# Kernel tuning notes

Measured on AMD Instinct MI355X. Metric: run time of the kernel, lower is better.

The kernel has to match this reference:

```python
import jax, jax.numpy as jnp
import numpy as np

B, HI, WI, CV, CT, T = 8, 64, 64, 512, 512, 77
HH, DH = 8, 64
TOP_M, TOPP, CLAMP_LOGIT, TAU, ALPHA0 = 5, 0.9, 2.0, 0.5, 0.1


def setup_inputs() -> dict:
    key = jax.random.key(0)
    ks = jax.random.split(key, 12)
    s = 0.02
    w = lambda k, shp: jax.random.normal(k, shp, jnp.float32) * s
    return {
        "visual": jax.random.normal(ks[0], (B, HI, WI, CV), jnp.float32),
        "text": jax.random.normal(ks[1], (B, T, CT), jnp.float32),
        "ln1_g": jnp.ones((CV,), jnp.float32), "ln1_b": jnp.zeros((CV,), jnp.float32),
        "ln2_g": jnp.ones((CV,), jnp.float32), "ln2_b": jnp.zeros((CV,), jnp.float32),
        "Wq": w(ks[2], (CV, CV)), "bq": jnp.zeros((CV,), jnp.float32),
        "Wk": w(ks[3], (CT, CV)), "bk": jnp.zeros((CV,), jnp.float32),
        "Wv": w(ks[4], (CT, CV)), "bv": jnp.zeros((CV,), jnp.float32),
        "Wo": w(ks[5], (CV, CV)), "bo": jnp.zeros((CV,), jnp.float32),
        "Wg": w(ks[6], (CV, 1)), "bg": jnp.zeros((1,), jnp.float32),
        "W1": w(ks[7], (CV, 4 * CV)), "b1": jnp.zeros((4 * CV,), jnp.float32),
        "W2": w(ks[8], (4 * CV, CV)), "b2": jnp.zeros((CV,), jnp.float32),
        "logit_scale": jnp.asarray(np.log(1.0 / 0.07), jnp.float32),
        "alpha": jnp.asarray(ALPHA0, jnp.float32),
    }


def _ln(x, g, b, eps=1e-5):
    m = x.mean(-1, keepdims=True)
    v = ((x - m) ** 2).mean(-1, keepdims=True)
    return (x - m) * jax.lax.rsqrt(v + eps) * g + b


def _l2norm(t, eps=1e-6):  # F.normalize: x / max(||x||, eps)
    return t / jnp.maximum(jnp.linalg.norm(t, axis=-1, keepdims=True), eps)


def _sam_forward(visual, text, ln1_g, ln1_b, ln2_g, ln2_b, Wq, bq, Wk, bk, Wv, bv,
                 Wo, bo, Wg, bg, W1, b1, W2, b2, logit_scale, alpha):
    Bx, Hi, Wi, C = visual.shape
    N = Hi * Wi
    x = _ln(visual, ln1_g, ln1_b).reshape(Bx, N, C)          # pre-LN, [B,N,Cv]
    q_full = x @ Wq + bq
    k_full = text @ Wk + bk
    v_full = text @ Wv + bv
    pad = jnp.abs(text).sum(-1) <= 1e-6                      # [B,T] all-zero tokens
    q = _l2norm(q_full).reshape(Bx, N, HH, DH)               # normalize over full Cv, then split heads
    k = _l2norm(k_full).reshape(Bx, -1, HH, DH)
    v = v_full.reshape(Bx, -1, HH, DH)
    scale = jnp.exp(jnp.clip(logit_scale, -CLAMP_LOGIT, CLAMP_LOGIT)) / jnp.sqrt(jnp.float32(DH))
    sim = jnp.einsum("bnhd,bthd->bnht", q, k) * scale        # [B,N,H,T]
    sim = jnp.where(pad[:, None, None, :], -jnp.inf, sim)
    # top-m sparsify (keep entries >= kth largest)
    if TOP_M < sim.shape[-1]:
        kth = jax.lax.top_k(sim, TOP_M)[0][..., -1:]
        sim = jnp.where(sim >= kth, sim, -jnp.inf)
    attn = jax.nn.softmax(sim, axis=-1)
    # top-p nucleus: sort desc, keep cum<=p (always keep top-1), scatter back, renorm
    idx = jnp.argsort(-attn, axis=-1)
    prob = jnp.take_along_axis(attn, idx, axis=-1)
    keep = (jnp.cumsum(prob, axis=-1) <= TOPP).astype(attn.dtype)
    keep = keep.at[..., 0].set(1.0)
    inv = jnp.argsort(idx, axis=-1)
    sparse = jnp.take_along_axis(keep * prob, inv, axis=-1)
    attn = sparse / jnp.maximum(sparse.sum(-1, keepdims=True), 1e-6)
    # entropy-based confidence, [B,N,1]
    ah = attn.transpose(0, 2, 1, 3)                          # [B,H,N,T]
    maxp = ah.max(-1, keepdims=True)
    t_eff = jnp.maximum((ah > 0).astype(attn.dtype).sum(-1, keepdims=True), 1.0)
    denom = jnp.log(jnp.maximum(t_eff, 2.0))
    pc = jnp.maximum(ah, 1e-8)
    entropy = -(pc * jnp.log(pc)).sum(-1, keepdims=True) / denom
    conf = jnp.clip(maxp * (1.0 - entropy), 0.0, 1.0).mean(axis=1)
    aligned = jnp.einsum("bnht,bthd->bnhd", attn, v).reshape(Bx, N, C)
    aligned = aligned @ Wo + bo
    # trust region: cap ||aligned|| at tau * rms(x)
    x_rms = jnp.sqrt((x ** 2).mean(-1, keepdims=True)) + 1e-6
    a_norm = jnp.sqrt((aligned ** 2).sum(-1, keepdims=True))
    aligned = aligned * jnp.minimum(TAU * x_rms / jnp.maximum(a_norm, 1e-6), 1.0)
    gate = jax.nn.sigmoid(x @ Wg + bg) * conf
    y = x + alpha * gate * aligned
    h = jax.nn.gelu(_ln(y, ln2_g, ln2_b) @ W1 + b1, approximate=False)
    y = y + (h @ W2 + b2)
    return y.reshape(Bx, Hi, Wi, C)


def reference(visual, text, ln1_g, ln1_b, ln2_g, ln2_b, Wq, bq, Wk, bk, Wv, bv,
              Wo, bo, Wg, bg, W1, b1, W2, b2, logit_scale, alpha):
    return _sam_forward(visual, text, ln1_g, ln1_b, ln2_g, ln2_b, Wq, bq, Wk, bk,
                        Wv, bv, Wo, bo, Wg, bg, W1, b1, W2, b2, logit_scale, alpha)
```

## Files before the change

### kernel.cpp

```cpp
#include <hip/hip_runtime.h>
#include <hip/hip_bf16.h>
#include <math.h>

#define NROW 32768
#define CVC  512
#define T77  77
#define BT   616
#define HHC  8
#define DHC  64

typedef __attribute__((ext_vector_type(8))) short bf16x8;
typedef __attribute__((ext_vector_type(4))) float f32x4;

__device__ __forceinline__ void gload_lds16(const void* g, void* l) {
  __builtin_amdgcn_global_load_lds(
      (__attribute__((address_space(1))) void*)g,
      (__attribute__((address_space(3))) void*)l, 16, 0, 0);
}

__device__ __forceinline__ float wave_reduce_sum(float v) {
  #pragma unroll
  for (int s = 32; s > 0; s >>= 1) v += __shfl_xor(v, s, 64);
  return v;
}

__global__ __launch_bounds__(256)
void stats1_kernel(const float* __restrict__ visual, const float* __restrict__ g,
                   const float* __restrict__ b, const float* __restrict__ Wg,
                   const float* __restrict__ bg,
                   float* __restrict__ mean1, float* __restrict__ rstd1,
                   float* __restrict__ xrms, float* __restrict__ gpre,
                   __hip_bfloat16* __restrict__ xbf) {
  const int lane = threadIdx.x & 63;
  const int row  = blockIdx.x * 4 + (threadIdx.x >> 6);
  const float* vr = visual + (size_t)row * CVC + lane * 8;
  float4 va = *(const float4*)vr;
  float4 vb = *(const float4*)(vr + 4);
  float v[8] = {va.x, va.y, va.z, va.w, vb.x, vb.y, vb.z, vb.w};
  float s = 0.f;
  #pragma unroll
  for (int i = 0; i < 8; i++) s += v[i];
  float m = wave_reduce_sum(s) * (1.0f / CVC);
  float s2 = 0.f;
  #pragma unroll
  for (int i = 0; i < 8; i++) { float d = v[i] - m; s2 += d * d; }
  float rs = rsqrtf(wave_reduce_sum(s2) * (1.0f / CVC) + 1e-5f);
  const float4 g0 = *(const float4*)(g + lane * 8), g1v = *(const float4*)(g + lane * 8 + 4);
  const float4 b0 = *(const float4*)(b + lane * 8), b1v = *(const float4*)(b + lane * 8 + 4);
  const float4 w0 = *(const float4*)(Wg + lane * 8), w1 = *(const float4*)(Wg + lane * 8 + 4);
  float gg[8] = {g0.x, g0.y, g0.z, g0.w, g1v.x, g1v.y, g1v.z, g1v.w};
  float bb[8] = {b0.x, b0.y, b0.z, b0.w, b1v.x, b1v.y, b1v.z, b1v.w};
  float ww[8] = {w0.x, w0.y, w0.z, w0.w, w1.x, w1.y, w1.z, w1.w};
  float x[8], sx2 = 0.f, sg = 0.f;
  union { bf16x8 v8; __hip_bfloat16 h[8]; } u;
  #pragma unroll
  for (int i = 0; i < 8; i++) {
    x[i] = (v[i] - m) * rs * gg[i] + bb[i];
    sx2 += x[i] * x[i];
    sg  += x[i] * ww[i];
    u.h[i] = __float2bfloat16(x[i]);
  }
  *(bf16x8*)(xbf + (size_t)row * CVC + lane * 8) = u.v8;
  sx2 = wave_reduce_sum(sx2);
  sg  = wave_reduce_sum(sg);
  if (lane == 0) {
    mean1[row] = m; rstd1[row] = rs;
    xrms[row] = sqrtf(sx2 * (1.0f / CVC)) + 1e-6f;
    gpre[row] = sg + bg[0];
  }
}

__global__ void convT_kernel(const float* __restrict__ W, __hip_bfloat16* __restrict__ Wt,
                             int K, int N) {
  __shared__ float t[32][33];
  int n0 = blockIdx.x * 32, k0 = blockIdx.y * 32;
  int tx = threadIdx.x, ty = threadIdx.y;
  #pragma unroll
  for (int i = 0; i < 32; i += 8) t[ty + i][tx] = W[(size_t)(k0 + ty + i) * N + n0 + tx];
  __syncthreads();
  #pragma unroll
  for (int i = 0; i < 32; i += 8)
    Wt[(size_t)(n0 + ty + i) * K + k0 + tx] = __float2bfloat16(t[tx][ty + i]);
}

template<int EPI>
__global__ __launch_bounds__(512, 2)
void mfma_gemm(const __hip_bfloat16* __restrict__ A, const __hip_bfloat16* __restrict__ Bt,
               const float* __restrict__ bias, float* __restrict__ out,
               __hip_bfloat16* __restrict__ outbf, int M, int N, int K) {
  __shared__ __align__(16) char lds[131072];
  const int tid = threadIdx.x;
  const int lane = tid & 63;
  const int wid  = tid >> 6;

  const int nwg  = gridDim.x * gridDim.y;
  const int orig = blockIdx.y * gridDim.x + blockIdx.x;
  const int wg   = (orig & 7) * (nwg >> 3) + (orig >> 3);
  const int bx = wg % gridDim.x;
  const int by = wg / gridDim.x;
  const int bm = by * 256, bn = bx * 256;

  const int wm = wid >> 2, wn = wid & 3;
  const int lrow = lane & 15, kq = lane >> 4;

  f32x4 acc[8][4] = {};

  const int r_in = lane >> 3;
  const int cblk = (lane & 7) ^ r_in;
  const __hip_bfloat16* gA = A  + (size_t)(bm + r_in) * K + cblk * 8;
  const __hip_bfloat16* gB = Bt + (size_t)(bn + r_in) * K + cblk * 8;
  char* ldsA = lds;
  char* ldsB = lds + 65536;

  auto stageA = [&](int buf, int k0, int half) {
    #pragma unroll
    for (int j = 0; j < 2; j++) {
      int R0 = half * 128 + wid * 16 + j * 8;
      gload_lds16(gA + (size_t)R0 * K + k0, ldsA + buf * 32768 + R0 * 128);
    }
  };
  auto stageB = [&](int buf, int k0, int half) {
    #pragma unroll
    for (int j = 0; j < 2; j++) {
      int R0 = half * 128 + wid * 16 + j * 8;
      gload_lds16(gB + (size_t)R0 * K + k0, ldsB + buf * 32768 + R0 * 128);
    }
  };

  const int swz = lrow & 7;
  auto ldA = [&](int buf, int m, int kk) -> bf16x8 {
    int r = wm * 128 + m * 16 + lrow;
    int blk = (kk * 4 + kq) ^ swz;
    return *(const bf16x8*)(ldsA + buf * 32768 + r * 128 + blk * 16);
  };
  auto ldB = [&](int buf, int n, int kk) -> bf16x8 {
    int r = wn * 64 + n * 16 + lrow;
    int blk = (kk * 4 + kq) ^ swz;
    return *(const bf16x8*)(ldsB + buf * 32768 + r * 128 + blk * 16);
  };

  const int NT = K >> 6;
  stageB(0, 0, 0); stageB(0, 0, 1);
  stageA(0, 0, 0); stageA(0, 0, 1);
  stageB(1, 64, 0); stageB(1, 64, 1);

  bf16x8 af[4][2], bfv[4][2];
  for (int t = 0; t < NT; ++t) {
    const int cur = t & 1;
    if (t < NT - 1) {
      asm volatile("s_waitcnt vmcnt(4)" ::: "memory");
    } else {
      asm volatile("s_waitcnt vmcnt(0)" ::: "memory");
    }
    __builtin_amdgcn_s_barrier();
    asm volatile("" ::: "memory");

    #pragma unroll
    for (int m = 0; m < 4; m++) { af[m][0] = ldA(cur, m, 0); af[m][1] = ldA(cur, m, 1); }
    #pragma unroll
    for (int n = 0; n < 2; n++) { bfv[n][0] = ldB(cur, n, 0); bfv[n][1] = ldB(cur, n, 1); }
    if (t + 1 < NT) stageA(cur ^ 1, (t + 1) << 6, 0);
    __builtin_amdgcn_s_setprio(1);
    #pragma unroll
    for (int m = 0; m < 4; m++)
      #pragma unroll
      for (int n = 0; n < 2; n++) {
        acc[m][n] = __builtin_amdgcn_mfma_f32_16x16x32_bf16(af[m][0], bfv[n][0], acc[m][n], 0, 0, 0);
        acc[m][n] = __builtin_amdgcn_mfma_f32_16x16x32_bf16(af[m][1], bfv[n][1], acc[m][n], 0, 0, 0);
      }
    __builtin_amdgcn_s_setprio(0);

    #pragma unroll
    for (int n = 2; n < 4; n++) { bfv[n][0] = ldB(cur, n, 0); bfv[n][1] = ldB(cur, n, 1); }
    if (t + 1 < NT) stageA(cur ^ 1, (t + 1) << 6, 1);
    __builtin_amdgcn_s_setprio(1);
    #pragma unroll
    for (int m = 0; m < 4; m++)
      #pragma unroll
      for (int n = 2; n < 4; n++) {
        acc[m][n] = __builtin_amdgcn_mfma_f32_16x16x32_bf16(af[m][0], bfv[n][0], acc[m][n], 0, 0, 0);
        acc[m][n] = __builtin_amdgcn_mfma_f32_16x16x32_bf16(af[m][1], bfv[n][1], acc[m][n], 0, 0, 0);
      }
    __builtin_amdgcn_s_setprio(0);

    asm volatile("s_waitcnt lgkmcnt(0)" ::: "memory");
    __builtin_amdgcn_s_barrier();
    asm volatile("" ::: "memory");

    #pragma unroll
    for (int m = 0; m < 4; m++) { af[m][0] = ldA(cur, m + 4, 0); af[m][1] = ldA(cur, m + 4, 1); }
    if (t + 2 < NT) stageB(cur, (t + 2) << 6, 0);
    __builtin_amdgcn_s_setprio(1);
    #pragma unroll
    for (int m = 0; m < 4; m++)
      #pragma unroll
      for (int n = 0; n < 2; n++) {
        acc[m + 4][n] = __builtin_amdgcn_mfma_f32_16x16x32_bf16(af[m][0], bfv[n][0], acc[m + 4][n], 0, 0, 0);
        acc[m + 4][n] = __builtin_amdgcn_mfma_f32_16x16x32_bf16(af[m][1], bfv[n][1], acc[m + 4][n], 0, 0, 0);
      }
    __builtin_amdgcn_s_setprio(0);

    if (t + 2 < NT) stageB(cur, (t + 2) << 6, 1);
    __builtin_amdgcn_s_setprio(1);
    #pragma unroll
    for (int m = 0; m < 4; m++)
      #pragma unroll
      for (int n = 2; n < 4; n++) {
        acc[m + 4][n] = __builtin_amdgcn_mfma_f32_16x16x32_bf16(af[m][0], bfv[n][0], acc[m + 4][n], 0, 0, 0);
        acc[m + 4][n] = __builtin_amdgcn_mfma_f32_16x16x32_bf16(af[m][1], bfv[n][1], acc[m + 4][n], 0, 0, 0);
      }
    __builtin_amdgcn_s_setprio(0);
  }

  const int c0 = bn + wn * 64 + lrow;
  if (EPI == 1) {
    __syncthreads();
    char* eb = lds + wid * 16384;
    #pragma unroll
    for (int n = 0; n < 4; n++) {
      float bval = bias[c0 + n * 16];
      #pragma unroll
      for (int m = 0; m < 8; m++) {
        #pragma unroll
        for (int rg = 0; rg < 4; rg++) {
          int lr  = m * 16 + kq * 4 + rg;
          int lcb = (n * 32 + lrow * 2) ^ (kq << 5);
          float v = acc[m][n][rg] + bval;
          float ge = v / (1.0f + __expf(v * (-1.5957691216f - 0.0713548162f * v * v)));
          *(__hip_bfloat16*)(eb + lr * 128 + lcb) = __float2bfloat16(ge);
        }
      }
    }
    asm volatile("s_waitcnt lgkmcnt(0)" ::: "memory");
    __builtin_amdgcn_sched_barrier(0);
    const int rr = lane >> 3, bb = lane & 7;
    #pragma unroll
    for (int it = 0; it < 16; it++) {
      int lr  = it * 8 + rr;
      int lcb = (bb << 4) ^ (((lr >> 2) & 3) << 5);
      uint4 v = *(const uint4*)(eb + lr * 128 + lcb);
      size_t go = (size_t)(bm + wm * 128 + lr) * N + (bn + wn * 64 + bb * 8);
      *(uint4*)(&outbf[go]) = v;
    }
  } else {
    __syncthreads();
    char* eb = lds + wid * 16384;
    const int rr = lane >> 4, bb = lane & 15;
    #pragma unroll
    for (int half = 0; half < 2; half++) {
      if (half) {
        asm volatile("s_waitcnt lgkmcnt(0)" ::: "memory");
        __builtin_amdgcn_sched_barrier(0);
      }
      #pragma unroll
      for (int n = 0; n < 4; n++) {
        float bval = bias[c0 + n * 16];
        #pragma unroll
        for (int m = 0; m < 4; m++) {
          #pragma unroll
          for (int rg = 0; rg < 4; rg++) {
            int lr  = m * 16 + kq * 4 + rg;
            int byo = (n * 64 + lrow * 4) ^ (kq << 6);
            *(float*)(eb + lr * 256 + byo) = acc[half * 4 + m][n][rg] + bval;
          }
        }
      }
      asm volatile("s_waitcnt lgkmcnt(0)" ::: "memory");
      __builtin_amdgcn_sched_barrier(0);
      #pragma unroll
      for (int it = 0; it < 16; it++) {
        int lr  = it * 4 + rr;
        int byo = (bb * 16) ^ (((lr >> 2) & 3) << 6);
        float4 v4 = *(const float4*)(eb + lr * 256 + byo);
        size_t go = (size_t)(bm + wm * 128 + half * 64 + lr) * N + (bn + wn * 64 + bb * 4);
        if (EPI == 0) {
          *(float4*)(&out[go]) = v4;
        } else {
          const float4 o = *(const float4*)(&out[go]);
          v4.x += o.x; v4.y += o.y; v4.z += o.z; v4.w += o.w;
          *(float4*)(&out[go]) = v4;
        }
      }
    }
  }
}

__global__ void kv2_gemm(const float* __restrict__ A,
                         const float* __restrict__ Wk, const float* __restrict__ bk,
                         const float* __restrict__ Wv, const float* __restrict__ bv,
                         float* __restrict__ KF, float* __restrict__ VF,
                         int M, int K, int N) {
  __shared__ float As[16][68];
  __shared__ float Bs[16][68];
  const bool isV = blockIdx.y >= 10;
  const float* W    = isV ? Wv : Wk;
  const float* bias = isV ? bv : bk;
  float* out        = isV ? VF : KF;
  int tid = threadIdx.x;
  int bm = (isV ? blockIdx.y - 10 : blockIdx.y) * 64, bn = blockIdx.x * 64;
  int ty = tid >> 4, tx = tid & 15;
  float acc[4][4] = {};
  for (int k0 = 0; k0 < K; k0 += 16) {
    #pragma unroll
    for (int i = 0; i < 4; i++) {
      int idx = tid + i * 256;
      int mm = idx >> 4, kk = idx & 15;
      int row = bm + mm;
      As[kk][mm] = (row < M) ? A[(size_t)row * K + k0 + kk] : 0.f;
    }
    #pragma unroll
    for (int i = 0; i < 4; i++) {
      int idx = tid + i * 256;
      int kk = idx >> 6, nn = idx & 63;
      Bs[kk][nn] = W[(size_t)(k0 + kk) * N + bn + nn];
    }
    __syncthreads();
    #pragma unroll
    for (int kk = 0; kk < 16; kk++) {
      float4 av = *(const float4*)&As[kk][ty * 4];
      float4 bv4 = *(const float4*)&Bs[kk][tx * 4];
      float a_[4] = {av.x, av.y, av.z, av.w};
      float b_[4] = {bv4.x, bv4.y, bv4.z, bv4.w};
      #pragma unroll
      for (int i = 0; i < 4; i++)
        #pragma unroll
        for (int j = 0; j < 4; j++)
          acc[i][j] = fmaf(a_[i], b_[j], acc[i][j]);
    }
    __syncthreads();
  }
  #pragma unroll
  for (int i = 0; i < 4; i++) {
    int row = bm + ty * 4 + i;
    if (row >= M) continue;
    #pragma unroll
    for (int j = 0; j < 4; j++) {
      int col = bn + tx * 4 + j;
      out[(size_t)row * N + col] = acc[i][j] + bias[col];
    }
  }
}

__global__ __launch_bounds__(256)
void l2norm_kernel(const float* __restrict__ buf, __hip_bfloat16* __restrict__ qbf) {
  const int lane = threadIdx.x & 63;
  const int row  = blockIdx.x * 4 + (threadIdx.x >> 6);
  const float* p = buf + (size_t)row * CVC + lane * 8;
  float4 va = *(const float4*)p;
  float4 vb = *(const float4*)(p + 4);
  float v[8] = {va.x, va.y, va.z, va.w, vb.x, vb.y, vb.z, vb.w};
  float s = 0.f;
  #pragma unroll
  for (int i = 0; i < 8; i++) s += v[i] * v[i];
  s = wave_reduce_sum(s);
  float inv = 1.0f / fmaxf(sqrtf(s), 1e-6f);
  union { bf16x8 v8; __hip_bfloat16 h[8]; } u;
  #pragma unroll
  for (int i = 0; i < 8; i++) u.h[i] = __float2bfloat16(v[i] * inv);
  *(bf16x8*)(qbf + (size_t)row * CVC + lane * 8) = u.v8;
}

__global__ __launch_bounds__(256)
void knorm_kernel(float* __restrict__ kf, const float* __restrict__ text,
                  int* __restrict__ pad) {
  const int lane = threadIdx.x & 63;
  const int row  = blockIdx.x * 4 + (threadIdx.x >> 6);
  float* p = kf + (size_t)row * CVC + lane * 8;
  const float* tx = text + (size_t)row * CVC + lane * 8;
  float4 va = *(const float4*)p;
  float4 vb = *(const float4*)(p + 4);
  float4 ta = *(const float4*)tx;
  float4 tb = *(const float4*)(tx + 4);
  float v[8] = {va.x, va.y, va.z, va.w, vb.x, vb.y, vb.z, vb.w};
  float t[8] = {ta.x, ta.y, ta.z, ta.w, tb.x, tb.y, tb.z, tb.w};
  float s = 0.f, a = 0.f;
  #pragma unroll
  for (int i = 0; i < 8; i++) { s += v[i] * v[i]; a += fabsf(t[i]); }
  s = wave_reduce_sum(s);
  a = wave_reduce_sum(a);
  float inv = 1.0f / fmaxf(sqrtf(s), 1e-6f);
  float4 o0 = {v[0] * inv, v[1] * inv, v[2] * inv, v[3] * inv};
  float4 o1 = {v[4] * inv, v[5] * inv, v[6] * inv, v[7] * inv};
  *(float4*)p = o0;
  *(float4*)(p + 4) = o1;
  if (lane == 0) pad[row] = (a <= 1e-6f) ? 1 : 0;
}

__global__ void kbf_kernel(const float* __restrict__ kf, __hip_bfloat16* __restrict__ kbf) {
  int bh = blockIdx.x;
  int b = bh >> 3, h = bh & 7;
  int tid = threadIdx.x;
  for (int i = tid; i < 80 * 64; i += 256) {
    int t = i >> 6, d = i & 63;
    float v = (t < T77) ? kf[(size_t)(b * T77 + t) * CVC + h * DHC + d] : 0.0f;
    kbf[(size_t)bh * (80 * 64) + i] = __float2bfloat16(v);
  }
}

__global__ __launch_bounds__(256)
void simA_kernel(const __hip_bfloat16* __restrict__ qbf, const __hip_bfloat16* __restrict__ kbf,
                 float* __restrict__ sim) {
  const int tid = threadIdx.x;
  const int wid = tid >> 6, lane = tid & 63;
  const int r0 = blockIdx.x * 64 + wid * 16;
  const int b = (blockIdx.x * 64) >> 12;
  const int lrow = lane & 15, kq = lane >> 4;
  const __hip_bfloat16* qrow = qbf + (size_t)(r0 + lrow) * CVC;
  for (int h = 0; h < HHC; h++) {
    const __hip_bfloat16* kb = kbf + (size_t)(b * 8 + h) * (80 * 64);
    f32x4 acc[5] = {};
    #pragma unroll
    for (int ks = 0; ks < 2; ks++) {
      bf16x8 af = *(const bf16x8*)(qrow + h * DHC + ks * 32 + kq * 8);
      #pragma unroll
      for (int n = 0; n < 5; n++) {
        bf16x8 bf = *(const bf16x8*)(kb + (size_t)(n * 16 + lrow) * DHC + ks * 32 + kq * 8);
        acc[n] = __builtin_amdgcn_mfma_f32_16x16x32_bf16(af, bf, acc[n], 0, 0, 0);
      }
    }
    #pragma unroll
    for (int n = 0; n < 5; n++)
      #pragma unroll
      for (int rg = 0; rg < 4; rg++)
        sim[(size_t)(r0 + kq * 4 + rg) * 640 + h * 80 + n * 16 + lrow] = acc[n][rg];
  }
}

__global__ __launch_bounds__(256)
void attnB_kernel(const float* __restrict__ sim, const float* __restrict__ vf,
                  const int* __restrict__ pad, const float* __restrict__ ls,
                  float* __restrict__ conf_out, __hip_bfloat16* __restrict__ abf) {
  __shared__ float spr[32][HHC][5];
  __shared__ int   sti[32][HHC][5];
  __shared__ float sconf[256];
  __shared__ float sbias[80];
  const int tid = threadIdx.x;
  const int r = tid >> 3, h = tid & 7;
  const int r0 = blockIdx.x * 32;
  const int b = r0 >> 12;
  const float lsv = fminf(fmaxf(ls[0], -2.0f), 2.0f);
  const float scale = expf(lsv) * 0.125f;

  if (tid < 80) sbias[tid] = (tid < T77 && !pad[b * T77 + tid]) ? 0.0f : -INFINITY;
  __syncthreads();

  float t0 = -INFINITY, t1 = -INFINITY, t2 = -INFINITY, t3 = -INFINITY, t4 = -INFINITY;
  int   i0 = -1, i1 = -1, i2 = -1, i3 = -1, i4 = -1;
  const float4* simp = (const float4*)(sim + (size_t)(r0 + r) * 640 + h * 80);
  #pragma unroll
  for (int tt = 0; tt < 20; tt++) {
    float4 v4 = simp[tt];
    #pragma unroll
    for (int j = 0; j < 4; j++) {
      int t = tt * 4 + j;
      float sv = (j == 0 ? v4.x : j == 1 ? v4.y : j == 2 ? v4.z : v4.w);
      float s = sv * scale + sbias[t];
      if (s > t4) {
        t4 = s; i4 = t;
        if (t4 > t3) { float f = t3; t3 = t4; t4 = f; int x = i3; i3 = i4; i4 = x; }
        if (t3 > t2) { float f = t2; t2 = t3; t3 = f; int x = i2; i2 = i3; i3 = x; }
        if (t2 > t1) { float f = t1; t1 = t2; t2 = f; int x = i1; i1 = i2; i2 = x; }
        if (t1 > t0) { float f = t0; t0 = t1; t1 = f; int x = i0; i0 = i1; i1 = x; }
      }
    }
  }

  float e0 = (t0 == -INFINITY) ? 0.f : expf(t0 - t0);
  float e1 = (t1 == -INFINITY) ? 0.f : expf(t1 - t0);
  float e2 = (t2 == -INFINITY) ? 0.f : expf(t2 - t0);
  float e3 = (t3 == -INFINITY) ? 0.f : expf(t3 - t0);
  float e4 = (t4 == -INFINITY) ? 0.f : expf(t4 - t0);
  float invs = 1.0f / (e0 + e1 + e2 + e3 + e4);
  float p0 = e0 * invs, p1 = e1 * invs, p2 = e2 * invs, p3 = e3 * invs, p4 = e4 * invs;
  float c1 = p0 + p1, c2 = c1 + p2, c3 = c2 + p3, c4 = c3 + p4;
  bool k1 = (c1 <= 0.9f), k2 = (c2 <= 0.9f), k3 = (c3 <= 0.9f), k4 = (c4 <= 0.9f);
  float skeep = p0 + (k1 ? p1 : 0.f) + (k2 ? p2 : 0.f) + (k3 ? p3 : 0.f) + (k4 ? p4 : 0.f);
  float rn = 1.0f / fmaxf(skeep, 1e-6f);
  float w0 = p0 * rn, w1 = k1 ? p1 * rn : 0.f, w2 = k2 ? p2 * rn : 0.f,
        w3 = k3 ? p3 * rn : 0.f, w4 = k4 ? p4 * rn : 0.f;
  int nnz = (w0 > 0.f) + (w1 > 0.f) + (w2 > 0.f) + (w3 > 0.f) + (w4 > 0.f);
  float ent = 0.f;
  {
    float pc;
    pc = fmaxf(w0, 1e-8f); ent -= pc * logf(pc);
    pc = fmaxf(w1, 1e-8f); ent -= pc * logf(pc);
    pc = fmaxf(w2, 1e-8f); ent -= pc * logf(pc);
    pc = fmaxf(w3, 1e-8f); ent -= pc * logf(pc);
    pc = fmaxf(w4, 1e-8f); ent -= pc * logf(pc);
  }
  ent += (float)(T77 - 5) * 1.8420681e-7f;
  float denom = logf(fmaxf(fmaxf((float)nnz, 1.0f), 2.0f));
  ent /= denom;
  float confh = fminf(fmaxf(w0 * (1.0f - ent), 0.f), 1.f);

  spr[r][h][0] = w0; spr[r][h][1] = w1; spr[r][h][2] = w2; spr[r][h][3] = w3; spr[r][h][4] = w4;
  sti[r][h][0] = i0; sti[r][h][1] = i1; sti[r][h][2] = i2; sti[r][h][3] = i3; sti[r][h][4] = i4;
  sconf[tid] = confh;
  __syncthreads();

  if (tid < 32) {
    float s = 0.f;
    #pragma unroll
    for (int j = 0; j < 8; j++) s += sconf[tid * 8 + j];
    conf_out[r0 + tid] = s * 0.125f;
  }

  #pragma unroll
  for (int it = 0; it < 64; it++) {
    int idx = tid + it * 256;
    int rr = idx >> 9, c = idx & 511, hh = c >> 6;
    float a = 0.f;
    #pragma unroll
    for (int i = 0; i < 5; i++) {
      float pr = spr[rr][hh][i]; int t = sti[rr][hh][i];
      if (pr > 0.f && t >= 0) a = fmaf(pr, vf[((size_t)(b * T77 + t)) * CVC + c], a);
    }
    abf[(size_t)(r0 + rr) * CVC + c] = __float2bfloat16(a);
  }
}

__global__ __launch_bounds__(256)
void combine_kernel(const float* __restrict__ al1, const float* __restrict__ visual,
                    const float* __restrict__ m1, const float* __restrict__ r1,
                    const float* __restrict__ g1, const float* __restrict__ b1v,
                    const float* __restrict__ xrms, const float* __restrict__ gpre,
                    const float* __restrict__ conf, const float* __restrict__ alpha,
                    const float* __restrict__ g2, const float* __restrict__ b2v,
                    float* __restrict__ dout, __hip_bfloat16* __restrict__ ybf) {
  const int lane = threadIdx.x & 63;
  const int row  = blockIdx.x * 4 + (threadIdx.x >> 6);
  const float* ar = al1 + (size_t)row * CVC + lane * 8;
  float4 aa = *(const float4*)ar;
  float4 ab = *(const float4*)(ar + 4);
  float av[8] = {aa.x, aa.y, aa.z, aa.w, ab.x, ab.y, ab.z, ab.w};
  float s2 = 0.f;
  #pragma unroll
  for (int i = 0; i < 8; i++) s2 += av[i] * av[i];
  s2 = wave_reduce_sum(s2);
  float an = sqrtf(s2);
  float factor = fminf(0.5f * xrms[row] / fmaxf(an, 1e-6f), 1.0f);
  float gate = conf[row] / (1.0f + expf(-gpre[row]));
  float coef = alpha[0] * gate * factor;
  float mm = m1[row], rs = r1[row];
  const float* vr = visual + (size_t)row * CVC + lane * 8;
  float4 va = *(const float4*)vr;
  float4 vb = *(const float4*)(vr + 4);
  float v[8] = {va.x, va.y, va.z, va.w, vb.x, vb.y, vb.z, vb.w};
  const float4 ga = *(const float4*)(g1 + lane * 8), gb = *(const float4*)(g1 + lane * 8 + 4);
  const float4 ba = *(const float4*)(b1v + lane * 8), bb2 = *(const float4*)(b1v + lane * 8 + 4);
  float gg[8] = {ga.x, ga.y, ga.z, ga.w, gb.x, gb.y, gb.z, gb.w};
  float bbv[8] = {ba.x, ba.y, ba.z, ba.w, bb2.x, bb2.y, bb2.z, bb2.w};
  float y[8], sy = 0.f;
  #pragma unroll
  for (int i = 0; i < 8; i++) {
    float x = (v[i] - mm) * rs * gg[i] + bbv[i];
    y[i] = x + coef * av[i];
    sy += y[i];
  }
  float* orow = dout + (size_t)row * CVC + lane * 8;
  float4 o0 = {y[0], y[1], y[2], y[3]};
  float4 o1 = {y[4], y[5], y[6], y[7]};
  *(float4*)orow = o0;
  *(float4*)(orow + 4) = o1;
  float ym = wave_reduce_sum(sy) * (1.0f / CVC);
  float var = 0.f;
  #pragma unroll
  for (int i = 0; i < 8; i++) { float d = y[i] - ym; var += d * d; }
  var = wave_reduce_sum(var) * (1.0f / CVC);
  float rs2 = rsqrtf(var + 1e-5f);
  const float4 g2a = *(const float4*)(g2 + lane * 8), g2b = *(const float4*)(g2 + lane * 8 + 4);
  const float4 b2a = *(const float4*)(b2v + lane * 8), b2b = *(const float4*)(b2v + lane * 8 + 4);
  float g2v[8] = {g2a.x, g2a.y, g2a.z, g2a.w, g2b.x, g2b.y, g2b.z, g2b.w};
  float b2vv[8] = {b2a.x, b2a.y, b2a.z, b2a.w, b2b.x, b2b.y, b2b.z, b2b.w};
  union { bf16x8 v8; __hip_bfloat16 h[8]; } u;
  #pragma unroll
  for (int i = 0; i < 8; i++)
    u.h[i] = __float2bfloat16((y[i] - ym) * rs2 * g2v[i] + b2vv[i]);
  *(bf16x8*)(ybf + (size_t)row * CVC + lane * 8) = u.v8;
}

extern "C" void kernel_launch(void* const* d_in, const int* in_sizes, int n_in,
                              void* d_out, int out_size, void* d_ws, size_t ws_size,
                              hipStream_t stream) {
  const float* visual = (const float*)d_in[0];
  const float* text   = (const float*)d_in[1];
  const float* ln1_g  = (const float*)d_in[2];
  const float* ln1_b  = (const float*)d_in[3];
  const float* ln2_g  = (const float*)d_in[4];
  const float* ln2_b  = (const float*)d_in[5];
  const float* Wq = (const float*)d_in[6];  const float* bq = (const float*)d_in[7];
  const float* Wk = (const float*)d_in[8];  const float* bk = (const float*)d_in[9];
  const float* Wv = (const float*)d_in[10]; const float* bv = (const float*)d_in[11];
  const float* Wo = (const float*)d_in[12]; const float* bo = (const float*)d_in[13];
  const float* Wg = (const float*)d_in[14]; const float* bg = (const float*)d_in[15];
  const float* W1 = (const float*)d_in[16]; const float* b1 = (const float*)d_in[17];
  const float* W2 = (const float*)d_in[18]; const float* b2 = (const float*)d_in[19];
  const float* ls    = (const float*)d_in[20];
  const float* alpha = (const float*)d_in[21];
  float* out = (float*)d_out;

  char* base = (char*)d_ws;
  __hip_bfloat16* H   = (__hip_bfloat16*)base;
  float* BUFA = (float*)base;
  float* SIM  = (float*)base;
  float* BUFB = (float*)(base + ((size_t)64 << 20));
  __hip_bfloat16* CBF = (__hip_bfloat16*)(base + ((size_t)128 << 20));
  char* p = base + ((size_t)160 << 20);
  __hip_bfloat16* WqT = (__hip_bfloat16*)p; p += (size_t)512 * 512 * 2;
  __hip_bfloat16* WoT = (__hip_bfloat16*)p; p += (size_t)512 * 512 * 2;
  __hip_bfloat16* W1T = (__hip_bfloat16*)p; p += (size_t)2048 * 512 * 2;
  __hip_bfloat16* W2T = (__hip_bfloat16*)p; p += (size_t)512 * 2048 * 2;
  float* KF = (float*)p; p += (size_t)BT * CVC * 4;
  float* VF = (float*)p; p += (size_t)BT * CVC * 4;
  int* PADF = (int*)p;  p += 4096;
  float* MEAN1 = (float*)p; p += (size_t)NROW * 4;
  float* RSTD1 = (float*)p; p += (size_t)NROW * 4;
  float* XRMS  = (float*)p; p += (size_t)NROW * 4;
  float* GPRE  = (float*)p; p += (size_t)NROW * 4;
  float* CONF  = (float*)p; p += (size_t)NROW * 4;
  __hip_bfloat16* KBF = (__hip_bfloat16*)p; p += (size_t)64 * 80 * 64 * 2;

  stats1_kernel<<<NROW / 4, 256, 0, stream>>>(visual, ln1_g, ln1_b, Wg, bg,
                                              MEAN1, RSTD1, XRMS, GPRE, CBF);
  convT_kernel<<<dim3(16, 16), dim3(32, 8), 0, stream>>>(Wq, WqT, 512, 512);
  convT_kernel<<<dim3(16, 16), dim3(32, 8), 0, stream>>>(Wo, WoT, 512, 512);
  convT_kernel<<<dim3(64, 16), dim3(32, 8), 0, stream>>>(W1, W1T, 512, 2048);
  convT_kernel<<<dim3(16, 64), dim3(32, 8), 0, stream>>>(W2, W2T, 2048, 512);

  mfma_gemm<0><<<dim3(2, 128), 512, 0, stream>>>(CBF, WqT, bq, BUFA, nullptr, NROW, 512, 512);
  l2norm_kernel<<<NROW / 4, 256, 0, stream>>>(BUFA, CBF);

  kv2_gemm<<<dim3(8, 20), 256, 0, stream>>>(text, Wk, bk, Wv, bv, KF, VF, BT, CVC, CVC);
  knorm_kernel<<<BT / 4, 256, 0, stream>>>(KF, text, PADF);
  kbf_kernel<<<64, 256, 0, stream>>>(KF, KBF);

  simA_kernel<<<NROW / 64, 256, 0, stream>>>(CBF, KBF, SIM);
  attnB_kernel<<<NROW / 32, 256, 0, stream>>>(SIM, VF, PADF, ls, CONF, CBF);

  mfma_gemm<0><<<dim3(2, 128), 512, 0, stream>>>(CBF, WoT, bo, BUFB, nullptr, NROW, 512, 512);

  combine_kernel<<<NROW / 4, 256, 0, stream>>>(BUFB, visual, MEAN1, RSTD1, ln1_g, ln1_b,
                                               XRMS, GPRE, CONF, alpha, ln2_g, ln2_b, out, CBF);

  mfma_gemm<1><<<dim3(8, 128), 512, 0, stream>>>(CBF, W1T, b1, nullptr, H, NROW, 2048, 512);

  mfma_gemm<2><<<dim3(2, 128), 512, 0, stream>>>(H, W2T, b2, out, nullptr, NROW, 512, 2048);
}
```

Before: 533.6 us.

## Restructure GEMM main loop into ping-pong schedule with per-quadrant barriers

The K loop of the MFMA GEMM is unrolled by two so the LDS buffer index is a compile-time constant. Each iteration is split into four quadrant phases, each fenced by extra s_barrier pairs. This resembles a ping-pong schedule where wave groups alternate between LDS reads/global staging and MFMA bursts. It aims to better overlap memory traffic with matrix math, at the cost of many more barriers, and it assumes NT is even.

```diff
diff --git a/kernel.cpp b/kernel.cpp
--- a/kernel.cpp
+++ b/kernel.cpp
@@ -139,78 +139,81 @@
     return *(const bf16x8*)(ldsB + buf * 32768 + r * 128 + blk * 16);
   };
 
-  const int NT = K >> 6;
+  const int NT  = K >> 6;
+  const int NIT = NT >> 1;
   stageB(0, 0, 0); stageB(0, 0, 1);
   stageA(0, 0, 0); stageA(0, 0, 1);
   stageB(1, 64, 0); stageB(1, 64, 1);
-
-  bf16x8 af[4][2], bfv[4][2];
-  for (int t = 0; t < NT; ++t) {
-    const int cur = t & 1;
-    if (t < NT - 1) {
-      asm volatile("s_waitcnt vmcnt(4)" ::: "memory");
-    } else {
-      asm volatile("s_waitcnt vmcnt(0)" ::: "memory");
-    }
-    __builtin_amdgcn_s_barrier();
-    asm volatile("" ::: "memory");
-
-    #pragma unroll
-    for (int m = 0; m < 4; m++) { af[m][0] = ldA(cur, m, 0); af[m][1] = ldA(cur, m, 1); }
-    #pragma unroll
-    for (int n = 0; n < 2; n++) { bfv[n][0] = ldB(cur, n, 0); bfv[n][1] = ldB(cur, n, 1); }
-    if (t + 1 < NT) stageA(cur ^ 1, (t + 1) << 6, 0);
-    __builtin_amdgcn_s_setprio(1);
-    #pragma unroll
-    for (int m = 0; m < 4; m++)
-      #pragma unroll
-      for (int n = 0; n < 2; n++) {
-        acc[m][n] = __builtin_amdgcn_mfma_f32_16x16x32_bf16(af[m][0], bfv[n][0], acc[m][n], 0, 0, 0);
-        acc[m][n] = __builtin_amdgcn_mfma_f32_16x16x32_bf16(af[m][1], bfv[n][1], acc[m][n], 0, 0, 0);
-      }
-    __builtin_amdgcn_s_setprio(0);
-
-    #pragma unroll
-    for (int n = 2; n < 4; n++) { bfv[n][0] = ldB(cur, n, 0); bfv[n][1] = ldB(cur, n, 1); }
-    if (t + 1 < NT) stageA(cur ^ 1, (t + 1) << 6, 1);
-    __builtin_amdgcn_s_setprio(1);
-    #pragma unroll
-    for (int m = 0; m < 4; m++)
-      #pragma unroll
-      for (int n = 2; n < 4; n++) {
-        acc[m][n] = __builtin_amdgcn_mfma_f32_16x16x32_bf16(af[m][0], bfv[n][0], acc[m][n], 0, 0, 0);
-        acc[m][n] = __builtin_amdgcn_mfma_f32_16x16x32_bf16(af[m][1], bfv[n][1], acc[m][n], 0, 0, 0);
-      }
-    __builtin_amdgcn_s_setprio(0);
-
-    asm volatile("s_waitcnt lgkmcnt(0)" ::: "memory");
-    __builtin_amdgcn_s_barrier();
-    asm volatile("" ::: "memory");
-
-    #pragma unroll
-    for (int m = 0; m < 4; m++) { af[m][0] = ldA(cur, m + 4, 0); af[m][1] = ldA(cur, m + 4, 1); }
-    if (t + 2 < NT) stageB(cur, (t + 2) << 6, 0);
-    __builtin_amdgcn_s_setprio(1);
-    #pragma unroll
-    for (int m = 0; m < 4; m++)
-      #pragma unroll
-      for (int n = 0; n < 2; n++) {
-        acc[m + 4][n] = __builtin_amdgcn_mfma_f32_16x16x32_bf16(af[m][0], bfv[n][0], acc[m + 4][n], 0, 0, 0);
-        acc[m + 4][n] = __builtin_amdgcn_mfma_f32_16x16x32_bf16(af[m][1], bfv[n][1], acc[m + 4][n], 0, 0, 0);
-      }
-    __builtin_amdgcn_s_setprio(0);
-
-    if (t + 2 < NT) stageB(cur, (t + 2) << 6, 1);
-    __builtin_amdgcn_s_setprio(1);
-    #pragma unroll
-    for (int m = 0; m < 4; m++)
-      #pragma unroll
-      for (int n = 2; n < 4; n++) {
-        acc[m + 4][n] = __builtin_amdgcn_mfma_f32_16x16x32_bf16(af[m][0], bfv[n][0], acc[m + 4][n], 0, 0, 0);
-        acc[m + 4][n] = __builtin_amdgcn_mfma_f32_16x16x32_bf16(af[m][1], bfv[n][1], acc[m + 4][n], 0, 0, 0);
-      }
-    __builtin_amdgcn_s_setprio(0);
-  }
+  asm volatile("s_waitcnt vmcnt(4)" ::: "memory");
+  __builtin_amdgcn_s_barrier();
+
+  bf16x8 af[4][2], bf01[2][2], bf23[2][2];
+
+  auto rdAf = [&](int buf, int mb) {
+    #pragma unroll
+    for (int m = 0; m < 4; m++) { af[m][0] = ldA(buf, mb + m, 0); af[m][1] = ldA(buf, mb + m, 1); }
+  };
+  auto rdB01 = [&](int buf) {
+    #pragma unroll
+    for (int n = 0; n < 2; n++) { bf01[n][0] = ldB(buf, n, 0); bf01[n][1] = ldB(buf, n, 1); }
+  };
+  auto rdB23 = [&](int buf) {
+    #pragma unroll
+    for (int n = 0; n < 2; n++) { bf23[n][0] = ldB(buf, n + 2, 0); bf23[n][1] = ldB(buf, n + 2, 1); }
+  };
+
+#define QUAD(MB, NB, BFX) \
+  __builtin_amdgcn_s_setprio(1); \
+  _Pragma("unroll") \
+  for (int m = 0; m < 4; m++) { \
+    _Pragma("unroll") \
+    for (int n = 0; n < 2; n++) { \
+      acc[(MB)+m][(NB)+n] = __builtin_amdgcn_mfma_f32_16x16x32_bf16(af[m][0], BFX[n][0], acc[(MB)+m][(NB)+n], 0, 0, 0); \
+      acc[(MB)+m][(NB)+n] = __builtin_amdgcn_mfma_f32_16x16x32_bf16(af[m][1], BFX[n][1], acc[(MB)+m][(NB)+n], 0, 0, 0); \
+    } \
+  } \
+  __builtin_amdgcn_s_setprio(0);
+#define BARR  __builtin_amdgcn_s_barrier()
+#define LGKM0 asm volatile("s_waitcnt lgkmcnt(0)" ::: "memory")
+#define LGKM8 asm volatile("s_waitcnt lgkmcnt(8)" ::: "memory")
+
+  for (int i = 0; i < NIT; ++i) {
+    const int u   = 2 * i;
+    const bool nl = (i + 1 < NIT);
+    const int kv  = (u + 1) << 6;
+    const int ku2 = (u + 2) << 6;
+    const int kv2 = (u + 3) << 6;
+
+    rdAf(0, 0); rdB01(0);
+    stageA(1, kv, 0);
+    LGKM8; BARR; LGKM0; QUAD(0, 0, bf01); BARR;
+    rdB23(0);
+    stageA(1, kv, 1);
+    BARR; LGKM0; QUAD(0, 2, bf23); BARR;
+    rdAf(0, 4);
+    if (nl) stageB(0, ku2, 0);
+    BARR; LGKM0; QUAD(4, 0, bf01); BARR;
+    if (nl) { stageB(0, ku2, 1); asm volatile("s_waitcnt vmcnt(4)" ::: "memory"); }
+    else    { asm volatile("s_waitcnt vmcnt(0)" ::: "memory"); }
+    BARR; QUAD(4, 2, bf23); BARR;
+
+    rdAf(1, 0); rdB01(1);
+    if (nl) stageA(0, ku2, 0);
+    LGKM8; BARR; LGKM0; QUAD(0, 0, bf01); BARR;
+    rdB23(1);
+    if (nl) stageA(0, ku2, 1);
+    BARR; LGKM0; QUAD(0, 2, bf23); BARR;
+    rdAf(1, 4);
+    if (nl) stageB(1, kv2, 0);
+    BARR; LGKM0; QUAD(4, 0, bf01); BARR;
+    if (nl) { stageB(1, kv2, 1); asm volatile("s_waitcnt vmcnt(4)" ::: "memory"); }
+    else    { asm volatile("s_waitcnt vmcnt(0)" ::: "memory"); }
+    BARR; QUAD(4, 2, bf23); BARR;
+  }
+#undef QUAD
+#undef BARR
+#undef LGKM0
+#undef LGKM8
 
   const int c0 = bn + wn * 64 + lrow;
   if (EPI == 1) {
```

Measured after the change: 542.9 us. About the same (+1.7%).
